# Optimization experiments

Hardware: AMD Instinct MI355X
Metric: run time of the kernel (lower is better)

The kernel has to match this reference:

```python
import jax, jax.numpy as jnp
import numpy as np

B, A, C, G = 32, 8732, 201, 50
NEG_TO_POS_RATIO = 3
MIN_NEG_SAMPLES = 0
DET_W, VAL_W = 0.5, 0.5
BOX_W = (10.0, 10.0, 5.0, 5.0)  # torchvision SSD BoxCoder weights


def _rand_boxes(key, shape_prefix):
    k1, k2 = jax.random.split(key)
    cxcy = jax.random.uniform(k1, shape_prefix + (2,)) * 300.0
    wh = jax.random.uniform(k2, shape_prefix + (2,)) * 90.0 + 10.0
    return jnp.concatenate([cxcy - 0.5 * wh, cxcy + 0.5 * wh], axis=-1)


def setup_inputs() -> dict:
    key = jax.random.key(0)
    ks = jax.random.split(key, 8)
    boxes = _rand_boxes(ks[0], (B, G))
    labels = jax.random.randint(ks[1], (B, G), 1, C, dtype=jnp.int32)  # foreground labels > 0
    image_label = jax.random.randint(ks[2], (B,), 0, 2, dtype=jnp.int32)
    bbox_regression = jax.random.normal(ks[3], (B, A, 4), dtype=jnp.float32)
    cls_logits = jax.random.normal(ks[4], (B, A, C), dtype=jnp.float32)
    rejection_logits = jax.random.normal(ks[5], (B, 2), dtype=jnp.float32)
    anchors = _rand_boxes(ks[6], (B, A))
    k7a, k7b = jax.random.split(ks[7])
    fg = jax.random.uniform(k7a, (B, A)) < 0.02
    gt_idx = jax.random.randint(k7b, (B, A), 0, G, dtype=jnp.int32)
    matched_idxs = jnp.where(fg, gt_idx, -1).astype(jnp.int32)
    return {"boxes": boxes, "labels": labels, "image_label": image_label,
            "bbox_regression": bbox_regression, "cls_logits": cls_logits,
            "rejection_logits": rejection_logits, "anchors": anchors,
            "matched_idxs": matched_idxs}


def _encode(gt, anc):
    # torchvision BoxCoder.encode_single with weights (10,10,5,5); boxes are xyxy
    aw = anc[..., 2] - anc[..., 0]
    ah = anc[..., 3] - anc[..., 1]
    acx = anc[..., 0] + 0.5 * aw
    acy = anc[..., 1] + 0.5 * ah
    gw = gt[..., 2] - gt[..., 0]
    gh = gt[..., 3] - gt[..., 1]
    gcx = gt[..., 0] + 0.5 * gw
    gcy = gt[..., 1] + 0.5 * gh
    wx, wy, ww, wh = BOX_W
    return jnp.stack([wx * (gcx - acx) / aw,
                      wy * (gcy - acy) / ah,
                      ww * jnp.log(gw / aw),
                      wh * jnp.log(gh / ah)], axis=-1)


def _forward(boxes, bbox_regression, cls_logits, rejection_logits, anchors,
             labels, image_label, matched_idxs):
    fg = matched_idxs >= 0                                  # [B,A]
    safe = jnp.clip(matched_idxs, 0)                        # in-range gather idx
    num_foreground = fg.sum()

    mg_boxes = jnp.take_along_axis(boxes, safe[..., None], axis=1)  # [B,A,4]
    target_reg = _encode(mg_boxes, anchors)
    d = bbox_regression - target_reg
    ad = jnp.abs(d)
    sl1 = jnp.where(ad < 1.0, 0.5 * d * d, ad - 0.5)        # beta=1.0
    bbox_loss = jnp.sum(sl1 * fg[..., None].astype(sl1.dtype), axis=(1, 2))  # [B]

    # --- classification targets + per-anchor CE ---
    cls_targets = jnp.where(fg, jnp.take_along_axis(labels, safe, axis=1), 0)  # [B,A]
    logp = jax.nn.log_softmax(cls_logits, axis=-1)
    cls_loss = -jnp.take_along_axis(logp, cls_targets[..., None], axis=-1)[..., 0]  # [B,A]

    # --- hard negative mining via double-argsort ranking ---
    fg_mask = cls_targets > 0
    num_neg = NEG_TO_POS_RATIO * fg_mask.sum(axis=1, keepdims=True)
    num_neg = jnp.where(num_neg == 0, MIN_NEG_SAMPLES, num_neg)
    neg_loss = jnp.where(fg_mask, -jnp.inf, cls_loss)
    rank = jnp.argsort(jnp.argsort(-neg_loss, axis=1), axis=1)  # descending rank
    bg_mask = rank < num_neg

    N = jnp.maximum(1, num_foreground).astype(cls_loss.dtype)
    images_without_boxes = (cls_targets.sum(axis=1) == 0).sum()
    N_neg = (MIN_NEG_SAMPLES * images_without_boxes).astype(cls_loss.dtype)

    regression_loss = bbox_loss.sum() / N
    classification_loss = (jnp.sum(jnp.where(fg_mask, cls_loss, 0.0)) +
                           jnp.sum(jnp.where(bg_mask, cls_loss, 0.0))) / (N + N_neg)

    # --- validation head loss ---
    val_logp = jax.nn.log_softmax(rejection_logits, axis=-1)
    validation_loss = -jnp.take_along_axis(val_logp, image_label[:, None], axis=-1).mean()

    loss = DET_W * (regression_loss + classification_loss) + VAL_W * validation_loss
    return jnp.stack([loss, regression_loss, classification_loss, validation_loss])


def reference(boxes, labels, image_label, bbox_regression, cls_logits,
              rejection_logits, anchors, matched_idxs):
    return _forward(boxes, bbox_regression, cls_logits, rejection_logits, anchors,
                    labels, image_label, matched_idxs)
```

## Files before the change

kernel.cpp:

```cpp
#include <hip/hip_runtime.h>
#include <math.h>

#define Bn 32
#define An 8732
#define Cn 201
#define Gn 50

#define APB 16
#define CLS_BLOCKS ((An + APB - 1) / APB)

__device__ __forceinline__ unsigned int f2key(float f) {
    unsigned int u = __float_as_uint(f);
    return (u & 0x80000000u) ? ~u : (u | 0x80000000u);
}
__device__ __forceinline__ float key2f(unsigned int k) {
    return (k & 0x80000000u) ? __uint_as_float(k & 0x7FFFFFFFu) : __uint_as_float(~k);
}
__device__ __forceinline__ float smooth_l1(float d) {
    float ad = fabsf(d);
    return ad < 1.0f ? 0.5f * d * d : ad - 0.5f;
}

__global__ void init_kernel(int* fg_count, float* fg_cls_sum, float* bbox_sum) {
    int i = threadIdx.x;
    if (i < Bn) { fg_count[i] = 0; fg_cls_sum[i] = 0.f; bbox_sum[i] = 0.f; }
}

__global__ __launch_bounds__(256) void cls_kernel(
        const float* __restrict__ cls_logits,
        const int*   __restrict__ matched_idxs,
        const int*   __restrict__ labels,
        const float* __restrict__ boxes,
        const float* __restrict__ anchors,
        const float* __restrict__ bbox_regression,
        float* __restrict__ neg_loss,
        int*   __restrict__ fg_count,
        float* __restrict__ fg_cls_sum,
        float* __restrict__ bbox_sum) {
    int b   = blockIdx.y;
    int a   = blockIdx.x * APB + (threadIdx.x >> 4);
    int sub = threadIdx.x & 15;
    if (a >= An) return;
    size_t row_idx = (size_t)b * An + a;
    const float* lg = cls_logits + row_idx * Cn;

    float v[13];
    #pragma unroll
    for (int j = 0; j < 12; ++j) v[j] = lg[sub + 16 * j];
    bool has12 = (sub < Cn - 192);
    v[12] = has12 ? lg[sub + 192] : -INFINITY;

    float mx = v[0];
    #pragma unroll
    for (int j = 1; j < 13; ++j) mx = fmaxf(mx, v[j]);
    #pragma unroll
    for (int off = 8; off; off >>= 1) mx = fmaxf(mx, __shfl_xor(mx, off, 64));

    float s = 0.f;
    #pragma unroll
    for (int j = 0; j < 12; ++j) s += expf(v[j] - mx);
    if (has12) s += expf(v[12] - mx);
    #pragma unroll
    for (int off = 8; off; off >>= 1) s += __shfl_xor(s, off, 64);

    if (sub == 0) {
        float lse = mx + logf(s);
        int   mi  = matched_idxs[row_idx];
        bool  fg  = (mi >= 0);
        int   t   = fg ? labels[b * Gn + mi] : 0;
        float cl  = lse - lg[t];
        if (fg) {
            neg_loss[row_idx] = -INFINITY;
            atomicAdd(&fg_cls_sum[b], cl);
            atomicAdd(&fg_count[b], 1);
            const float* gt = boxes           + (size_t)(b * Gn + mi) * 4;
            const float* an = anchors         + row_idx * 4;
            const float* rg = bbox_regression + row_idx * 4;
            float aw  = an[2] - an[0], ah  = an[3] - an[1];
            float acx = an[0] + 0.5f * aw, acy = an[1] + 0.5f * ah;
            float gw  = gt[2] - gt[0], gh  = gt[3] - gt[1];
            float gcx = gt[0] + 0.5f * gw, gcy = gt[1] + 0.5f * gh;
            float t0 = 10.f * (gcx - acx) / aw;
            float t1 = 10.f * (gcy - acy) / ah;
            float t2 = 5.f * logf(gw / aw);
            float t3 = 5.f * logf(gh / ah);
            float sum = smooth_l1(rg[0] - t0) + smooth_l1(rg[1] - t1)
                      + smooth_l1(rg[2] - t2) + smooth_l1(rg[3] - t3);
            atomicAdd(&bbox_sum[b], sum);
        } else {
            neg_loss[row_idx] = cl;
        }
    }
}

#define MIT 9
__global__ __launch_bounds__(1024) void mining_kernel(
        const float* __restrict__ neg_loss,
        const int*   __restrict__ fg_count,
        float* __restrict__ topk_batch) {
    int b    = blockIdx.x;
    int tid  = threadIdx.x;
    int lane = tid & 63;
    __shared__ int   cnts[32];
    __shared__ float sh_sum;
    __shared__ int   sh_cnt;

    int fc = fg_count[b];
    int k  = 3 * fc;
    int nneg = An - fc;
    if (k > nneg) k = nneg;
    if (k <= 0) {
        if (tid == 0) topk_batch[b] = 0.f;
        return;
    }

    const float* vals = neg_loss + (size_t)b * An;
    unsigned int key[MIT];
    #pragma unroll
    for (int j = 0; j < MIT; ++j) {
        int i = tid + j * 1024;
        key[j] = (i < An) ? f2key(vals[i]) : 0u;
    }

    if (tid < 32) cnts[tid] = 0;
    if (tid == 0) { sh_sum = 0.f; sh_cnt = 0; }
    __syncthreads();

    unsigned int T = 0u;
    for (int bit = 31; bit >= 0; --bit) {
        unsigned int cand = T | (1u << bit);
        int c = 0;
        #pragma unroll
        for (int j = 0; j < MIT; ++j) c += (key[j] >= cand);
        #pragma unroll
        for (int off = 32; off; off >>= 1) c += __shfl_xor(c, off, 64);
        if (lane == 0) atomicAdd(&cnts[bit], c);
        __syncthreads();
        if (cnts[bit] >= k) T = cand;
    }

    float fs = 0.f; int cgt = 0;
    #pragma unroll
    for (int j = 0; j < MIT; ++j)
        if (key[j] > T) { fs += key2f(key[j]); cgt++; }
    #pragma unroll
    for (int off = 32; off; off >>= 1) {
        fs  += __shfl_xor(fs,  off, 64);
        cgt += __shfl_xor(cgt, off, 64);
    }
    if (lane == 0) { atomicAdd(&sh_sum, fs); atomicAdd(&sh_cnt, cgt); }
    __syncthreads();
    if (tid == 0)
        topk_batch[b] = sh_sum + (float)(k - sh_cnt) * key2f(T);
}

__global__ void finalize_kernel(
        const int*   __restrict__ fg_count,
        const float* __restrict__ fg_cls_sum,
        const float* __restrict__ bbox_sum,
        const float* __restrict__ topk_batch,
        const float* __restrict__ rejection_logits,
        const int*   __restrict__ image_label,
        float* __restrict__ out) {
    int lane = threadIdx.x;
    int   fc = (lane < Bn) ? fg_count[lane]   : 0;
    float tk = (lane < Bn) ? topk_batch[lane] : 0.f;
    float cs = (lane < Bn) ? fg_cls_sum[lane] : 0.f;
    float bs = (lane < Bn) ? bbox_sum[lane]   : 0.f;
    float vl = 0.f;
    if (lane < Bn) {
        float r0 = rejection_logits[lane * 2];
        float r1 = rejection_logits[lane * 2 + 1];
        float m  = fmaxf(r0, r1);
        float lse = m + logf(expf(r0 - m) + expf(r1 - m));
        vl = lse - ((image_label[lane] == 0) ? r0 : r1);
    }
    #pragma unroll
    for (int off = 32; off; off >>= 1) {
        fc += __shfl_xor(fc, off, 64);
        tk += __shfl_xor(tk, off, 64);
        cs += __shfl_xor(cs, off, 64);
        bs += __shfl_xor(bs, off, 64);
        vl += __shfl_xor(vl, off, 64);
    }
    if (lane == 0) {
        float N   = (float)((fc > 1) ? fc : 1);
        float reg = bs / N;
        float cls = (cs + tk) / N;
        float val = vl / (float)Bn;
        float loss = 0.5f * (reg + cls) + 0.5f * val;
        out[0] = loss; out[1] = reg; out[2] = cls; out[3] = val;
    }
}

extern "C" void kernel_launch(void* const* d_in, const int* in_sizes, int n_in,
                              void* d_out, int out_size, void* d_ws, size_t ws_size,
                              hipStream_t stream) {
    const float* boxes            = (const float*)d_in[0];
    const int*   labels           = (const int*)  d_in[1];
    const int*   image_label      = (const int*)  d_in[2];
    const float* bbox_regression  = (const float*)d_in[3];
    const float* cls_logits       = (const float*)d_in[4];
    const float* rejection_logits = (const float*)d_in[5];
    const float* anchors          = (const float*)d_in[6];
    const int*   matched_idxs     = (const int*)  d_in[7];
    float* out = (float*)d_out;

    float* neg_loss   = (float*)d_ws;
    int*   fg_count   = (int*)(neg_loss + Bn * An);
    float* fg_cls_sum = (float*)(fg_count + Bn);
    float* bbox_sum   = fg_cls_sum + Bn;
    float* topk_batch = bbox_sum + Bn;

    init_kernel<<<1, 64, 0, stream>>>(fg_count, fg_cls_sum, bbox_sum);

    dim3 grid(CLS_BLOCKS, Bn);
    cls_kernel<<<grid, 256, 0, stream>>>(cls_logits, matched_idxs, labels,
                                         boxes, anchors, bbox_regression,
                                         neg_loss, fg_count, fg_cls_sum, bbox_sum);

    mining_kernel<<<Bn, 1024, 0, stream>>>(neg_loss, fg_count, topk_batch);

    finalize_kernel<<<1, 64, 0, stream>>>(fg_count, fg_cls_sum, bbox_sum, topk_batch,
                                          rejection_logits, image_label, out);
}
```

Baseline: 349.7 us.

## Replace global atomics with per-block partials and radix-8 histogram top-k selection

The classification kernel stops using global atomics for per-image foreground sums. Each block now writes its partial cls and box sums, and the mining kernel reduces them and counts foregrounds by detecting the -inf key, which also removes the init kernel. The 32-pass bitwise threshold search becomes a 4-pass 8-bit radix histogram select that uses shared atomics and a wave prefix scan. exp is rewritten as exp2f. The intent is fewer barriers and passes in mining and no contended global atomics, at the cost of a more complex select with shared-histogram atomic contention.

```diff
diff --git a/kernel.cpp b/kernel.cpp
--- a/kernel.cpp
+++ b/kernel.cpp
@@ -8,6 +8,7 @@
 
 #define APB 16
 #define CLS_BLOCKS ((An + APB - 1) / APB)
+#define LOG2E 1.44269504088896340736f
 
 __device__ __forceinline__ unsigned int f2key(float f) {
     unsigned int u = __float_as_uint(f);
@@ -21,10 +22,7 @@
     return ad < 1.0f ? 0.5f * d * d : ad - 0.5f;
 }
 
-__global__ void init_kernel(int* fg_count, float* fg_cls_sum, float* bbox_sum) {
-    int i = threadIdx.x;
-    if (i < Bn) { fg_count[i] = 0; fg_cls_sum[i] = 0.f; bbox_sum[i] = 0.f; }
-}
+#define FGKEY 0x007FFFFFu
 
 __global__ __launch_bounds__(256) void cls_kernel(
         const float* __restrict__ cls_logits,
@@ -34,111 +32,168 @@
         const float* __restrict__ anchors,
         const float* __restrict__ bbox_regression,
         float* __restrict__ neg_loss,
-        int*   __restrict__ fg_count,
-        float* __restrict__ fg_cls_sum,
-        float* __restrict__ bbox_sum) {
+        float* __restrict__ part_cls,
+        float* __restrict__ part_box) {
+    __shared__ float shc[4], shb[4];
     int b   = blockIdx.y;
-    int a   = blockIdx.x * APB + (threadIdx.x >> 4);
+    int grp = threadIdx.x >> 4;
     int sub = threadIdx.x & 15;
-    if (a >= An) return;
-    size_t row_idx = (size_t)b * An + a;
-    const float* lg = cls_logits + row_idx * Cn;
-
-    float v[13];
-    #pragma unroll
-    for (int j = 0; j < 12; ++j) v[j] = lg[sub + 16 * j];
-    bool has12 = (sub < Cn - 192);
-    v[12] = has12 ? lg[sub + 192] : -INFINITY;
-
-    float mx = v[0];
-    #pragma unroll
-    for (int j = 1; j < 13; ++j) mx = fmaxf(mx, v[j]);
-    #pragma unroll
-    for (int off = 8; off; off >>= 1) mx = fmaxf(mx, __shfl_xor(mx, off, 64));
-
-    float s = 0.f;
-    #pragma unroll
-    for (int j = 0; j < 12; ++j) s += expf(v[j] - mx);
-    if (has12) s += expf(v[12] - mx);
-    #pragma unroll
-    for (int off = 8; off; off >>= 1) s += __shfl_xor(s, off, 64);
-
-    if (sub == 0) {
-        float lse = mx + logf(s);
-        int   mi  = matched_idxs[row_idx];
-        bool  fg  = (mi >= 0);
-        int   t   = fg ? labels[b * Gn + mi] : 0;
-        float cl  = lse - lg[t];
-        if (fg) {
-            neg_loss[row_idx] = -INFINITY;
-            atomicAdd(&fg_cls_sum[b], cl);
-            atomicAdd(&fg_count[b], 1);
-            const float* gt = boxes           + (size_t)(b * Gn + mi) * 4;
-            const float* an = anchors         + row_idx * 4;
-            const float* rg = bbox_regression + row_idx * 4;
-            float aw  = an[2] - an[0], ah  = an[3] - an[1];
-            float acx = an[0] + 0.5f * aw, acy = an[1] + 0.5f * ah;
-            float gw  = gt[2] - gt[0], gh  = gt[3] - gt[1];
-            float gcx = gt[0] + 0.5f * gw, gcy = gt[1] + 0.5f * gh;
-            float t0 = 10.f * (gcx - acx) / aw;
-            float t1 = 10.f * (gcy - acy) / ah;
-            float t2 = 5.f * logf(gw / aw);
-            float t3 = 5.f * logf(gh / ah);
-            float sum = smooth_l1(rg[0] - t0) + smooth_l1(rg[1] - t1)
-                      + smooth_l1(rg[2] - t2) + smooth_l1(rg[3] - t3);
-            atomicAdd(&bbox_sum[b], sum);
-        } else {
-            neg_loss[row_idx] = cl;
-        }
+    int a   = blockIdx.x * APB + grp;
+    bool valid = (a < An);
+    size_t row = (size_t)b * An + a;
+
+    float my_cl = 0.f, my_box = 0.f;
+    if (valid) {
+        const float* lg = cls_logits + row * (size_t)Cn;
+        float v[13];
+        #pragma unroll
+        for (int j = 0; j < 12; ++j) v[j] = lg[sub + 16 * j];
+        v[12] = (sub < Cn - 192) ? lg[sub + 192] : -INFINITY;
+
+        float mx = v[0];
+        #pragma unroll
+        for (int j = 1; j < 13; ++j) mx = fmaxf(mx, v[j]);
+        #pragma unroll
+        for (int off = 8; off; off >>= 1) mx = fmaxf(mx, __shfl_xor(mx, off, 64));
+
+        float s = 0.f;
+        #pragma unroll
+        for (int j = 0; j < 13; ++j) s += exp2f((v[j] - mx) * LOG2E);
+        #pragma unroll
+        for (int off = 8; off; off >>= 1) s += __shfl_xor(s, off, 64);
+
+        if (sub == 0) {
+            float lse = mx + logf(s);
+            int   mi  = matched_idxs[row];
+            bool  fg  = (mi >= 0);
+            int   t   = fg ? labels[b * Gn + mi] : 0;
+            float cl  = lse - lg[t];
+            if (fg) {
+                neg_loss[row] = -INFINITY;
+                my_cl = cl;
+                const float* gt = boxes           + (size_t)(b * Gn + mi) * 4;
+                const float* an = anchors         + row * 4;
+                const float* rg = bbox_regression + row * 4;
+                float aw  = an[2] - an[0], ah  = an[3] - an[1];
+                float acx = an[0] + 0.5f * aw, acy = an[1] + 0.5f * ah;
+                float gw  = gt[2] - gt[0], gh  = gt[3] - gt[1];
+                float gcx = gt[0] + 0.5f * gw, gcy = gt[1] + 0.5f * gh;
+                float t0 = 10.f * (gcx - acx) / aw;
+                float t1 = 10.f * (gcy - acy) / ah;
+                float t2 = 5.f * logf(gw / aw);
+                float t3 = 5.f * logf(gh / ah);
+                my_box = smooth_l1(rg[0] - t0) + smooth_l1(rg[1] - t1)
+                       + smooth_l1(rg[2] - t2) + smooth_l1(rg[3] - t3);
+            } else {
+                neg_loss[row] = cl;
+            }
+        }
+    }
+    my_cl  += __shfl_xor(my_cl, 16, 64);  my_cl  += __shfl_xor(my_cl, 32, 64);
+    my_box += __shfl_xor(my_box, 16, 64); my_box += __shfl_xor(my_box, 32, 64);
+    int wv = threadIdx.x >> 6, lane = threadIdx.x & 63;
+    if (lane == 0) { shc[wv] = my_cl; shb[wv] = my_box; }
+    __syncthreads();
+    if (threadIdx.x == 0) {
+        part_cls[b * CLS_BLOCKS + blockIdx.x] = shc[0] + shc[1] + shc[2] + shc[3];
+        part_box[b * CLS_BLOCKS + blockIdx.x] = shb[0] + shb[1] + shb[2] + shb[3];
     }
 }
 
 #define MIT 9
 __global__ __launch_bounds__(1024) void mining_kernel(
         const float* __restrict__ neg_loss,
-        const int*   __restrict__ fg_count,
+        const float* __restrict__ part_cls,
+        const float* __restrict__ part_box,
+        int*   __restrict__ fg_count,
+        float* __restrict__ fg_cls_sum,
+        float* __restrict__ bbox_sum,
         float* __restrict__ topk_batch) {
     int b    = blockIdx.x;
     int tid  = threadIdx.x;
     int lane = tid & 63;
-    __shared__ int   cnts[32];
-    __shared__ float sh_sum;
-    __shared__ int   sh_cnt;
-
-    int fc = fg_count[b];
-    int k  = 3 * fc;
-    int nneg = An - fc;
-    if (k > nneg) k = nneg;
-    if (k <= 0) {
-        if (tid == 0) topk_batch[b] = 0.f;
-        return;
-    }
+    int wv   = tid >> 6;
+    __shared__ int   h[256];
+    __shared__ float wfa[16], wfb[16];
+    __shared__ int   wia[16];
+    __shared__ unsigned int sh_prefix;
+    __shared__ int sh_krem, sh_k;
 
     const float* vals = neg_loss + (size_t)b * An;
     unsigned int key[MIT];
+    int myfg = 0;
     #pragma unroll
     for (int j = 0; j < MIT; ++j) {
         int i = tid + j * 1024;
-        key[j] = (i < An) ? f2key(vals[i]) : 0u;
-    }
-
-    if (tid < 32) cnts[tid] = 0;
-    if (tid == 0) { sh_sum = 0.f; sh_cnt = 0; }
-    __syncthreads();
-
-    unsigned int T = 0u;
-    for (int bit = 31; bit >= 0; --bit) {
-        unsigned int cand = T | (1u << bit);
-        int c = 0;
-        #pragma unroll
-        for (int j = 0; j < MIT; ++j) c += (key[j] >= cand);
-        #pragma unroll
-        for (int off = 32; off; off >>= 1) c += __shfl_xor(c, off, 64);
-        if (lane == 0) atomicAdd(&cnts[bit], c);
+        unsigned int kk = 0u;
+        if (i < An) { kk = f2key(vals[i]); myfg += (kk == FGKEY); }
+        key[j] = kk;
+    }
+    float mc = (tid < CLS_BLOCKS) ? part_cls[b * CLS_BLOCKS + tid] : 0.f;
+    float mb = (tid < CLS_BLOCKS) ? part_box[b * CLS_BLOCKS + tid] : 0.f;
+    #pragma unroll
+    for (int off = 32; off; off >>= 1) {
+        mc   += __shfl_xor(mc, off, 64);
+        mb   += __shfl_xor(mb, off, 64);
+        myfg += __shfl_xor(myfg, off, 64);
+    }
+    if (lane == 0) { wfa[wv] = mc; wfb[wv] = mb; wia[wv] = myfg; }
+    if (tid < 256) h[tid] = 0;
+    __syncthreads();
+    if (tid == 0) {
+        float cs = 0.f, bs = 0.f; int fc = 0;
+        for (int i = 0; i < 16; ++i) { cs += wfa[i]; bs += wfb[i]; fc += wia[i]; }
+        fg_count[b] = fc; fg_cls_sum[b] = cs; bbox_sum[b] = bs;
+        int k = 3 * fc, nneg = An - fc;
+        if (k > nneg) k = nneg;
+        sh_k = k; sh_krem = k; sh_prefix = 0u;
+    }
+    __syncthreads();
+    int k = sh_k;
+    if (k <= 0) { if (tid == 0) topk_batch[b] = 0.f; return; }
+
+    unsigned int prefix = 0; int krem = k;
+    for (int p = 0; p < 4; ++p) {
+        int shift = 24 - 8 * p;
+        #pragma unroll
+        for (int j = 0; j < MIT; ++j) {
+            unsigned int u = key[j];
+            bool match = (p == 0) || ((u >> (shift + 8)) == prefix);
+            if (match) atomicAdd(&h[(u >> shift) & 255], 1);
+        }
         __syncthreads();
-        if (cnts[bit] >= k) T = cand;
-    }
-
+        if (wv == 0) {
+            int b0 = 252 - 4 * lane;
+            int c0 = h[b0], c1 = h[b0 + 1], c2 = h[b0 + 2], c3 = h[b0 + 3];
+            int local = c0 + c1 + c2 + c3;
+            int inc = local;
+            #pragma unroll
+            for (int off = 1; off < 64; off <<= 1) {
+                int n = __shfl_up(inc, off, 64);
+                if (lane >= off) inc += n;
+            }
+            unsigned long long m = __ballot(inc >= krem);
+            int sel = __ffsll(m) - 1;
+            if (lane == sel) {
+                int prev = inc - local;
+                int digit, above;
+                if      (prev + c3 >= krem)           { digit = b0 + 3; above = prev; }
+                else if (prev + c3 + c2 >= krem)      { digit = b0 + 2; above = prev + c3; }
+                else if (prev + c3 + c2 + c1 >= krem) { digit = b0 + 1; above = prev + c3 + c2; }
+                else                                  { digit = b0;     above = prev + c3 + c2 + c1; }
+                sh_prefix = (prefix << 8) | (unsigned int)digit;
+                sh_krem   = krem - above;
+            }
+        }
+        __syncthreads();
+        prefix = sh_prefix; krem = sh_krem;
+        if (p < 3) {
+            if (tid < 256) h[tid] = 0;
+            __syncthreads();
+        }
+    }
+
+    unsigned int T = prefix;
     float fs = 0.f; int cgt = 0;
     #pragma unroll
     for (int j = 0; j < MIT; ++j)
@@ -148,10 +203,13 @@
         fs  += __shfl_xor(fs,  off, 64);
         cgt += __shfl_xor(cgt, off, 64);
     }
-    if (lane == 0) { atomicAdd(&sh_sum, fs); atomicAdd(&sh_cnt, cgt); }
-    __syncthreads();
-    if (tid == 0)
-        topk_batch[b] = sh_sum + (float)(k - sh_cnt) * key2f(T);
+    if (lane == 0) { wfa[wv] = fs; wia[wv] = cgt; }
+    __syncthreads();
+    if (tid == 0) {
+        float s = 0.f; int c = 0;
+        for (int i = 0; i < 16; ++i) { s += wfa[i]; c += wia[i]; }
+        topk_batch[b] = s + (float)(k - c) * key2f(T);
+    }
 }
 
 __global__ void finalize_kernel(
@@ -207,19 +265,20 @@
     float* out = (float*)d_out;
 
     float* neg_loss   = (float*)d_ws;
-    int*   fg_count   = (int*)(neg_loss + Bn * An);
+    float* part_cls   = neg_loss + (size_t)Bn * An;
+    float* part_box   = part_cls + Bn * CLS_BLOCKS;
+    int*   fg_count   = (int*)(part_box + Bn * CLS_BLOCKS);
     float* fg_cls_sum = (float*)(fg_count + Bn);
     float* bbox_sum   = fg_cls_sum + Bn;
     float* topk_batch = bbox_sum + Bn;
 
-    init_kernel<<<1, 64, 0, stream>>>(fg_count, fg_cls_sum, bbox_sum);
-
     dim3 grid(CLS_BLOCKS, Bn);
     cls_kernel<<<grid, 256, 0, stream>>>(cls_logits, matched_idxs, labels,
                                          boxes, anchors, bbox_regression,
-                                         neg_loss, fg_count, fg_cls_sum, bbox_sum);
-
-    mining_kernel<<<Bn, 1024, 0, stream>>>(neg_loss, fg_count, topk_batch);
+                                         neg_loss, part_cls, part_box);
+
+    mining_kernel<<<Bn, 1024, 0, stream>>>(neg_loss, part_cls, part_box,
+                                           fg_count, fg_cls_sum, bbox_sum, topk_batch);
 
     finalize_kernel<<<1, 64, 0, stream>>>(fg_count, fg_cls_sum, bbox_sum, topk_batch,
                                           rejection_logits, image_label, out);
```

New measurement: 334.5 us. -4.3%, faster.
